# Optimization experiments

Measured on AMD Instinct MI355X. Metric: run time of the kernel, lower is better.

## Reference

```python
import jax, jax.numpy as jnp
import numpy as np

RANK_W, SP_W, ANS_W = 1.0, 1.0, 1.0


def _listmle(thres, scores, labels):
    # thres [B,1], scores [B,P], labels [B,P] with values in {-1,0,1}
    fs = jnp.concatenate([thres, scores], axis=1)                      # [B,K]
    fl = jnp.concatenate([jnp.full_like(thres, 0.5), labels], axis=1)  # [B,K]
    s = jnp.exp(fs) * (fl != -1.0).astype(fs.dtype)
    # rest[b,j] = sum_k s[b,k] * (fl[b,k] < fl[b,j])  (sorting in the original
    # is only used to enumerate; with the 0.5 break it reduces to masking
    # entries with label >= 0.5)
    less = (fl[:, None, :] < fl[:, :, None]).astype(fs.dtype)          # [B,j,k]
    rest = jnp.einsum('bjk,bk->bj', less, s)
    mask = fl >= 0.5
    den = jnp.where(mask, s + rest, 1.0)
    logp = jnp.where(mask, fs - jnp.log(den), 0.0)  # log(s_j/(s_j+rest)) with s_j=exp(fs_j)
    return -jnp.sum(logp)


def setup_inputs() -> dict:
    key = jax.random.key(0)
    B, S, H, NS, NP, A = 8, 4096, 1024, 64, 32, 8
    ks = jax.random.split(key, 12)
    sequence_output = jax.random.normal(ks[0], (B, S, H), jnp.float32)
    token_type_ids = jax.random.randint(ks[1], (B, S), 0, 2).astype(jnp.int32)
    # strictly increasing sentence boundaries; last 4 sentences padded with -1
    base = jnp.round(jnp.linspace(8, S - 8, NS + 1)).astype(jnp.int32)
    sent_starts = jnp.broadcast_to(base, (B, NS + 1)).copy()
    sent_starts = sent_starts.at[:, -4:].set(-1)
    para_starts = jnp.sort(jax.random.randint(ks[2], (B, NP), 0, S), axis=1).astype(jnp.int32)
    para_labels = jax.random.randint(ks[3], (B, NP), -1, 2).astype(jnp.float32)
    sp_sent_labels = jax.random.randint(ks[4], (B, NS), -1, 2).astype(jnp.float32)
    starts = jax.random.randint(ks[5], (B, A), -1, S).astype(jnp.int32)
    ends = jax.random.randint(ks[6], (B, A), -1, S).astype(jnp.int32)
    Wqa = jax.random.normal(ks[7], (H, 2), jnp.float32) * 0.02
    bqa = jnp.zeros((2,), jnp.float32)
    Wrank = jax.random.normal(ks[8], (H, 1), jnp.float32) * 0.02
    brank = jnp.zeros((1,), jnp.float32)
    Wsp = jax.random.normal(ks[9], (H, 1), jnp.float32) * 0.02
    bsp = jnp.zeros((1,), jnp.float32)
    return {"sequence_output": sequence_output, "token_type_ids": token_type_ids,
            "sent_starts": sent_starts, "para_starts": para_starts,
            "para_labels": para_labels, "sp_sent_labels": sp_sent_labels,
            "starts": starts, "ends": ends, "Wqa": Wqa, "bqa": bqa,
            "Wrank": Wrank, "brank": brank, "Wsp": Wsp, "bsp": bsp}


def reference(sequence_output, token_type_ids, sent_starts, para_starts,
              para_labels, sp_sent_labels, starts, ends,
              Wqa, bqa, Wrank, brank, Wsp, bsp):
    B, S, H = sequence_output.shape
    logits = sequence_output @ Wqa + bqa                               # [B,S,2]
    tt1 = token_type_ids == 1
    start_logits = jnp.where(tt1, logits[..., 0], -jnp.inf)
    end_logits = jnp.where(tt1, logits[..., 1], -jnp.inf)

    rank_thres = sequence_output[:, 0, :] @ Wrank + brank              # [B,1]
    sent_thres = sequence_output[:, 0, :] @ Wsp + bsp                  # [B,1]

    # ragged per-sentence mean pooling via prefix sums
    csum = jnp.concatenate([jnp.zeros((B, 1, H), sequence_output.dtype),
                            jnp.cumsum(sequence_output, axis=1)], axis=1)  # [B,S+1,H]
    st = sent_starts[:, :-1]
    en = sent_starts[:, 1:]
    valid = en != -1                                                   # [B,NS]
    st_c = jnp.clip(st, 0, S)
    en_c = jnp.maximum(jnp.clip(en, 0, S), st_c + 1)
    NS = st.shape[1]
    g_en = jnp.take_along_axis(csum, jnp.broadcast_to(en_c[:, :, None], (B, NS, H)), axis=1)
    g_st = jnp.take_along_axis(csum, jnp.broadcast_to(st_c[:, :, None], (B, NS, H)), axis=1)
    seg_mean = (g_en - g_st) / (en_c - st_c)[:, :, None].astype(sequence_output.dtype)
    sent_rep = jnp.where(valid[:, :, None], seg_mean, sequence_output[:, -1:, :])
    sp_score = (sent_rep @ Wsp + bsp)[..., 0]                          # [B,NS]

    NP = para_starts.shape[1]
    para_rep = jnp.take_along_axis(
        sequence_output, jnp.broadcast_to(para_starts[:, :, None].astype(jnp.int32), (B, NP, H)), axis=1)
    para_score = (para_rep @ Wrank + brank)[..., 0]                    # [B,NP]

    rank_loss = _listmle(rank_thres, para_score, para_labels)
    sp_loss = _listmle(sent_thres, sp_score, sp_sent_labels)

    ls_start = jax.nn.log_softmax(start_logits, axis=-1)
    ls_end = jax.nn.log_softmax(end_logits, axis=-1)

    def ce(ls, tgt):  # CrossEntropy with ignore_index=-1, reduction='none'
        safe = jnp.clip(tgt, 0, S - 1)
        nll = -jnp.take_along_axis(ls, safe, axis=1)
        return jnp.where(tgt == -1, 0.0, nll)

    loss_tensor = ce(ls_start, starts) + ce(ls_end, ends)              # [B,A]
    lp = -loss_tensor
    lp = jnp.where(lp == 0.0, -jnp.inf, lp)
    m = jnp.sum(jnp.exp(lp), axis=1)                                   # [B]
    pos = m > 0
    span_loss = -jnp.sum(jnp.where(pos, jnp.log(jnp.where(pos, m, 1.0)), 0.0))

    loss = rank_loss * RANK_W + span_loss * ANS_W + sp_loss * SP_W
    return (loss, rank_loss * RANK_W, sp_loss * SP_W)
```

## Files before the change

kernel.cpp:

```cpp
#include <hip/hip_runtime.h>
#include <math.h>

#define B 8
#define S 4096
#define H 1024
#define NSEG 64
#define NPARA 32
#define NA 8
#define BS (B * S)
#define PAD(i) ((i) + ((i) >> 4))
#define ROWS_PER_BLK 16
#define GROUPS 4
#define BLKS_PER_B (S / ROWS_PER_BLK)
#define NBLK (B * BLKS_PER_B)

__device__ __forceinline__ void gload_lds16(const float4* g, float4* l)
{
    __builtin_amdgcn_global_load_lds(
        (const __attribute__((address_space(1))) void*)g,
        (__attribute__((address_space(3))) void*)l, 16, 0, 0);
}

__device__ __forceinline__ float2 lse_merge(float2 A, float2 Bv)
{
    float m = fmaxf(A.x, Bv.x);
    float s = 0.f;
    if (A.y > 0.f)  s += A.y * expf(A.x - m);
    if (Bv.y > 0.f) s += Bv.y * expf(Bv.x - m);
    return make_float2(m, s);
}

__global__ __launch_bounds__(256) void dots_kernel(
    const float4* __restrict__ seq4,
    const float*  __restrict__ Wqa,
    const float*  __restrict__ Wsp,
    const float*  __restrict__ Wrank,
    const int*    __restrict__ tt,
    float4* __restrict__ sc4,
    float4* __restrict__ lse_part,
    float*  __restrict__ out)
{
    const int blk   = blockIdx.x;
    const int b     = blk >> 8;
    const int rbase = (blk & 255) * ROWS_PER_BLK;
    const int t     = threadIdx.x;
    const int w     = t >> 6, lane = t & 63;

    if (blk == 0 && t == 0) { out[0] = 0.f; out[1] = 0.f; out[2] = 0.f; }

    __shared__ float4 sbuf[2][1024];
    __shared__ float4 lsep[4];

    float wq0[4][4], wq1[4][4];
    float4 wspv[4], wrkv[4];
#pragma unroll
    for (int c = 0; c < 4; ++c) {
        int h0 = (lane + 64 * c) * 4;
#pragma unroll
        for (int j = 0; j < 4; ++j) {
            wq0[c][j] = Wqa[(h0 + j) * 2 + 0];
            wq1[c][j] = Wqa[(h0 + j) * 2 + 1];
        }
        wspv[c] = *(const float4*)(Wsp + h0);
        wrkv[c] = *(const float4*)(Wrank + h0);
    }

    const size_t baseF4 = (size_t)(b * S + rbase) * (H / 4);
    const int    wbase  = t & ~63;

    {
        const float4* gsrc = seq4 + baseF4;
#pragma unroll
        for (int k = 0; k < 4; ++k)
            gload_lds16(gsrc + k * 256 + t, &sbuf[0][k * 256 + wbase]);
    }
    __syncthreads();

    const int* ttb = tt + b * S;
    float m0 = -INFINITY, s0 = 0.f, m1 = -INFINITY, s1 = 0.f;

    for (int g = 0; g < GROUPS; ++g) {
        if (g + 1 < GROUPS) {
            const float4* gsrc = seq4 + baseF4 + (size_t)(g + 1) * (4 * H / 4);
#pragma unroll
            for (int k = 0; k < 4; ++k)
                gload_lds16(gsrc + k * 256 + t, &sbuf[(g + 1) & 1][k * 256 + wbase]);
        }
        const float4* rowp = &sbuf[g & 1][w * 256];
        float a0 = 0.f, a1 = 0.f, a2 = 0.f, a3 = 0.f;
#pragma unroll
        for (int c = 0; c < 4; ++c) {
            float4 v = rowp[lane + 64 * c];
            a0 += v.x * wq0[c][0] + v.y * wq0[c][1] + v.z * wq0[c][2] + v.w * wq0[c][3];
            a1 += v.x * wq1[c][0] + v.y * wq1[c][1] + v.z * wq1[c][2] + v.w * wq1[c][3];
            a2 += v.x * wspv[c].x + v.y * wspv[c].y + v.z * wspv[c].z + v.w * wspv[c].w;
            a3 += v.x * wrkv[c].x + v.y * wrkv[c].y + v.z * wrkv[c].z + v.w * wrkv[c].w;
        }
#pragma unroll
        for (int off = 32; off > 0; off >>= 1) {
            a0 += __shfl_xor(a0, off);
            a1 += __shfl_xor(a1, off);
            a2 += __shfl_xor(a2, off);
            a3 += __shfl_xor(a3, off);
        }
        const int srow = rbase + g * 4 + w;
        if (ttb[srow] == 1) {
            float mn = fmaxf(m0, a0);
            s0 = s0 * expf(m0 - mn) + expf(a0 - mn); m0 = mn;
            mn = fmaxf(m1, a1);
            s1 = s1 * expf(m1 - mn) + expf(a1 - mn); m1 = mn;
        }
        if (lane == 0)
            sc4[b * S + srow] = make_float4(a0, a1, a2, a3);
        __syncthreads();
    }

    if (lane == 0) lsep[w] = make_float4(m0, s0, m1, s1);
    __syncthreads();
    if (t == 0) {
        float2 L0 = make_float2(lsep[0].x, lsep[0].y);
        float2 L1 = make_float2(lsep[0].z, lsep[0].w);
#pragma unroll
        for (int i = 1; i < 4; ++i) {
            L0 = lse_merge(L0, make_float2(lsep[i].x, lsep[i].y));
            L1 = lse_merge(L1, make_float2(lsep[i].z, lsep[i].w));
        }
        lse_part[blk] = make_float4(L0.x, L0.y, L1.x, L1.y);
    }
}

__device__ __forceinline__ float blk_reduce1(float v, float* wred1, int t)
{
    const int lane = t & 63, w = t >> 6;
#pragma unroll
    for (int off = 32; off > 0; off >>= 1) v += __shfl_xor(v, off);
    if (lane == 0) wred1[w] = v;
    __syncthreads();
    float r = wred1[0] + wred1[1] + wred1[2] + wred1[3];
    __syncthreads();
    return r;
}

__device__ float listmle_block(const float* fs, const float* fl, float* se,
                               int n, float* wred1, int t)
{
    if (t < n) se[t] = (fl[t] != -1.0f) ? expf(fs[t]) : 0.0f;
    __syncthreads();
    float lp = 0.0f;
    if (t < n && fl[t] >= 0.5f) {
        float fj = fl[t];
        float rest = 0.0f;
        for (int k = 0; k < n; ++k)
            if (fl[k] < fj) rest += se[k];
        lp = fs[t] - logf(se[t] + rest);
    }
    float tot = blk_reduce1(lp, wred1, t);
    return -tot;
}

__global__ __launch_bounds__(256) void batch_kernel(
    const float4* __restrict__ sc4,
    const float4* __restrict__ lse_part,
    const int*    __restrict__ tt,
    const int*    __restrict__ sent_starts,
    const int*    __restrict__ para_starts,
    const float*  __restrict__ para_labels,
    const float*  __restrict__ sp_labels,
    const int*    __restrict__ starts,
    const int*    __restrict__ ends,
    float* __restrict__ out)
{
    const int b = blockIdx.x;
    const int t = threadIdx.x;
    const int lane = t & 63, w = t >> 6;

    __shared__ float  a[PAD(S) + 1];
    __shared__ float4 lsew[4];
    __shared__ float  wred1[4];
    __shared__ float  fsb[1 + NSEG], flb[1 + NSEG], seb[1 + NSEG];
    __shared__ float  lse_sh[2];

    const float4* sb  = sc4 + (size_t)b * S;
    const int*    ttb = tt + b * S;

    {
        float4 P = lse_part[b * BLKS_PER_B + t];
        float2 L0 = make_float2(P.x, P.y);
        float2 L1 = make_float2(P.z, P.w);
#pragma unroll
        for (int off = 32; off > 0; off >>= 1) {
            float2 O0 = make_float2(__shfl_xor(L0.x, off), __shfl_xor(L0.y, off));
            float2 O1 = make_float2(__shfl_xor(L1.x, off), __shfl_xor(L1.y, off));
            L0 = lse_merge(L0, O0);
            L1 = lse_merge(L1, O1);
        }
        if (lane == 0) lsew[w] = make_float4(L0.x, L0.y, L1.x, L1.y);
        __syncthreads();
        if (t == 0) {
            float2 M0 = make_float2(lsew[0].x, lsew[0].y);
            float2 M1 = make_float2(lsew[0].z, lsew[0].w);
#pragma unroll
            for (int i = 1; i < 4; ++i) {
                M0 = lse_merge(M0, make_float2(lsew[i].x, lsew[i].y));
                M1 = lse_merge(M1, make_float2(lsew[i].z, lsew[i].w));
            }
            lse_sh[0] = M0.x + logf(M0.y);
            lse_sh[1] = M1.x + logf(M1.y);
        }
    }

    {
        for (int s = t; s < S; s += 256) a[PAD(s)] = sb[s].z;
        __syncthreads();
        float vals[16];
        float run = 0.f;
        const int base = t * 16;
#pragma unroll
        for (int i = 0; i < 16; ++i) {
            run += a[PAD(base + i)];
            vals[i] = run;
        }
        float v = run;
#pragma unroll
        for (int off = 1; off < 64; off <<= 1) {
            float u = __shfl_up(v, off, 64);
            if (lane >= off) v += u;
        }
        if (lane == 63) wred1[w] = v;
        __syncthreads();
        float woff = 0.f;
        for (int i = 0; i < w; ++i) woff += wred1[i];
        const float excl = woff + v - run;
        __syncthreads();
#pragma unroll
        for (int i = 0; i < 16; ++i) a[PAD(base + i + 1)] = excl + vals[i];
        if (t == 0) a[PAD(0)] = 0.f;
        __syncthreads();
    }

    if (t == 0) { fsb[0] = sb[0].z; flb[0] = 0.5f; }
    if (t < NSEG) {
        int st = sent_starts[b * (NSEG + 1) + t];
        int en = sent_starts[b * (NSEG + 1) + t + 1];
        int stc = min(max(st, 0), S);
        int enc = max(min(max(en, 0), S), stc + 1);
        float score;
        if (en != -1) {
            int encc = min(enc, S);
            score = (a[PAD(encc)] - a[PAD(stc)]) / (float)(enc - stc);
        } else {
            score = sb[S - 1].z;
        }
        fsb[1 + t] = score;
        flb[1 + t] = sp_labels[b * NSEG + t];
    }
    __syncthreads();
    float sp_loss_b = listmle_block(fsb, flb, seb, 1 + NSEG, wred1, t);

    if (t == 0) { fsb[0] = sb[0].w; flb[0] = 0.5f; }
    if (t < NPARA) {
        int ps = para_starts[b * NPARA + t];
        fsb[1 + t] = sb[ps].w;
        flb[1 + t] = para_labels[b * NPARA + t];
    }
    __syncthreads();
    float rank_loss_b = listmle_block(fsb, flb, seb, 1 + NPARA, wred1, t);

    float e_a = 0.f;
    if (t < NA) {
        const float lse0 = lse_sh[0], lse1 = lse_sh[1];
        int tsv = starts[b * NA + t];
        int tev = ends[b * NA + t];
        float lt = 0.f;
        if (tsv != -1) {
            int sf = min(max(tsv, 0), S - 1);
            float sl = (ttb[sf] == 1) ? sb[sf].x : -INFINITY;
            lt += -(sl - lse0);
        }
        if (tev != -1) {
            int sf = min(max(tev, 0), S - 1);
            float el = (ttb[sf] == 1) ? sb[sf].y : -INFINITY;
            lt += -(el - lse1);
        }
        float lp = -lt;
        e_a = (lp == 0.0f) ? 0.f : expf(lp);
    }
#pragma unroll
    for (int off = 4; off > 0; off >>= 1) e_a += __shfl_xor(e_a, off, 8);
    if (t == 0) {
        float logm = (e_a > 0.f) ? logf(e_a) : 0.f;
        atomicAdd(out + 0, rank_loss_b + sp_loss_b - logm);
        atomicAdd(out + 1, rank_loss_b);
        atomicAdd(out + 2, sp_loss_b);
    }
}

extern "C" void kernel_launch(void* const* d_in, const int* in_sizes, int n_in,
                              void* d_out, int out_size, void* d_ws, size_t ws_size,
                              hipStream_t stream)
{
    const float* seq         = (const float*)d_in[0];
    const int*   tt          = (const int*)  d_in[1];
    const int*   sent_starts = (const int*)  d_in[2];
    const int*   para_starts = (const int*)  d_in[3];
    const float* para_labels = (const float*)d_in[4];
    const float* sp_labels   = (const float*)d_in[5];
    const int*   starts      = (const int*)  d_in[6];
    const int*   ends        = (const int*)  d_in[7];
    const float* Wqa         = (const float*)d_in[8];
    const float* Wrank       = (const float*)d_in[10];
    const float* Wsp         = (const float*)d_in[12];

    float*  out      = (float*)d_out;
    float4* sc4      = (float4*)d_ws;
    float4* lse_part = sc4 + (size_t)BS;

    dots_kernel<<<NBLK, 256, 0, stream>>>((const float4*)seq, Wqa, Wsp, Wrank,
                                          tt, sc4, lse_part, out);
    batch_kernel<<<B, 256, 0, stream>>>(sc4, lse_part, tt, sent_starts,
                                        para_starts, para_labels, sp_labels,
                                        starts, ends, out);
}
```

Baseline: 40.82 us.

## Fuse segment sums into dots kernel and load rows via registers

The dots kernel now loads rows straight into registers with double buffering, replacing the async global-to-LDS copies and per-group barriers. Each block now covers 32 rows instead of 16. It maps each row to its sentence segment and emits per-block partial segment sums, so the batch kernel no longer needs its 4096-element prefix scan in LDS and only accumulates partials with shared atomics. This shortens the serial single-block-per-batch tail, at the cost of a small per-block segment search. It assumes each 32-row block spans at most two segments.

New measurement: 46.04 us. 1.13x slower.

```diff
diff --git a/kernel.cpp b/kernel.cpp
--- a/kernel.cpp
+++ b/kernel.cpp
@@ -8,18 +8,9 @@
 #define NPARA 32
 #define NA 8
 #define BS (B * S)
-#define PAD(i) ((i) + ((i) >> 4))
-#define ROWS_PER_BLK 16
-#define GROUPS 4
+#define ROWS_PER_BLK 32
 #define BLKS_PER_B (S / ROWS_PER_BLK)
 #define NBLK (B * BLKS_PER_B)
-
-__device__ __forceinline__ void gload_lds16(const float4* g, float4* l)
-{
-    __builtin_amdgcn_global_load_lds(
-        (const __attribute__((address_space(1))) void*)g,
-        (__attribute__((address_space(3))) void*)l, 16, 0, 0);
-}
 
 __device__ __forceinline__ float2 lse_merge(float2 A, float2 Bv)
 {
@@ -32,69 +23,91 @@
 
 __global__ __launch_bounds__(256) void dots_kernel(
     const float4* __restrict__ seq4,
-    const float*  __restrict__ Wqa,
-    const float*  __restrict__ Wsp,
-    const float*  __restrict__ Wrank,
+    const float4* __restrict__ Wqa4,
+    const float4* __restrict__ Wsp4,
+    const float4* __restrict__ Wrank4,
     const int*    __restrict__ tt,
+    const int*    __restrict__ sent_starts,
     float4* __restrict__ sc4,
     float4* __restrict__ lse_part,
+    float4* __restrict__ segpart,
     float*  __restrict__ out)
 {
     const int blk   = blockIdx.x;
-    const int b     = blk >> 8;
-    const int rbase = (blk & 255) * ROWS_PER_BLK;
+    const int b     = blk >> 7;
+    const int rbase = (blk & 127) * ROWS_PER_BLK;
     const int t     = threadIdx.x;
     const int w     = t >> 6, lane = t & 63;
 
     if (blk == 0 && t == 0) { out[0] = 0.f; out[1] = 0.f; out[2] = 0.f; }
 
-    __shared__ float4 sbuf[2][1024];
+    __shared__ int    ssh[NSEG + 1];
+    __shared__ int    rowseg[ROWS_PER_BLK];
+    __shared__ int    ttsh[ROWS_PER_BLK];
+    __shared__ float2 wacc[4];
     __shared__ float4 lsep[4];
-
-    float wq0[4][4], wq1[4][4];
-    float4 wspv[4], wrkv[4];
+    __shared__ int    jlo_sh;
+
+    float4 qA[4], qB[4], spv[4], rkv[4];
 #pragma unroll
     for (int c = 0; c < 4; ++c) {
-        int h0 = (lane + 64 * c) * 4;
-#pragma unroll
-        for (int j = 0; j < 4; ++j) {
-            wq0[c][j] = Wqa[(h0 + j) * 2 + 0];
-            wq1[c][j] = Wqa[(h0 + j) * 2 + 1];
-        }
-        wspv[c] = *(const float4*)(Wsp + h0);
-        wrkv[c] = *(const float4*)(Wrank + h0);
-    }
-
-    const size_t baseF4 = (size_t)(b * S + rbase) * (H / 4);
-    const int    wbase  = t & ~63;
-
-    {
-        const float4* gsrc = seq4 + baseF4;
-#pragma unroll
-        for (int k = 0; k < 4; ++k)
-            gload_lds16(gsrc + k * 256 + t, &sbuf[0][k * 256 + wbase]);
-    }
-    __syncthreads();
-
-    const int* ttb = tt + b * S;
+        const int ch = lane + 64 * c;
+        qA[c]  = Wqa4[ch * 2];
+        qB[c]  = Wqa4[ch * 2 + 1];
+        spv[c] = Wsp4[ch];
+        rkv[c] = Wrank4[ch];
+    }
+
+    if (t < NSEG + 1) ssh[t] = sent_starts[b * (NSEG + 1) + t];
+    __syncthreads();
+    if (t < ROWS_PER_BLK) {
+        ttsh[t] = tt[b * S + rbase + t];
+        const int r = rbase + t;
+        int j = -1;
+        for (int k = 0; k < NSEG; ++k) {
+            int en = ssh[k + 1];
+            if (en == -1) break;
+            if (r >= ssh[k] && r < en) { j = k; break; }
+        }
+        rowseg[t] = j;
+    }
+    __syncthreads();
+    if (t == 0) {
+        int jl = -1;
+        for (int i = 0; i < ROWS_PER_BLK; ++i)
+            if (rowseg[i] >= 0) { jl = rowseg[i]; break; }
+        jlo_sh = jl;
+    }
+    __syncthreads();
+    const int jlo = jlo_sh;
+
+    const float4* base = seq4 + (size_t)(b * S + rbase) * (H / 4);
+    float4 bufA[4], bufB[4];
+#pragma unroll
+    for (int c = 0; c < 4; ++c)
+        bufA[c] = base[(size_t)w * 256 + lane + 64 * c];
+
     float m0 = -INFINITY, s0 = 0.f, m1 = -INFINITY, s1 = 0.f;
-
-    for (int g = 0; g < GROUPS; ++g) {
-        if (g + 1 < GROUPS) {
-            const float4* gsrc = seq4 + baseF4 + (size_t)(g + 1) * (4 * H / 4);
-#pragma unroll
-            for (int k = 0; k < 4; ++k)
-                gload_lds16(gsrc + k * 256 + t, &sbuf[(g + 1) & 1][k * 256 + wbase]);
-        }
-        const float4* rowp = &sbuf[g & 1][w * 256];
+    float sA = 0.f, sB = 0.f;
+
+#pragma unroll
+    for (int g = 0; g < 8; ++g) {
+        const float4* cur = (g & 1) ? bufB : bufA;
+        float4*       nxt = (g & 1) ? bufA : bufB;
+        if (g + 1 < 8) {
+            const int nr = (g + 1) * 4 + w;
+#pragma unroll
+            for (int c = 0; c < 4; ++c)
+                nxt[c] = base[(size_t)nr * 256 + lane + 64 * c];
+        }
         float a0 = 0.f, a1 = 0.f, a2 = 0.f, a3 = 0.f;
 #pragma unroll
         for (int c = 0; c < 4; ++c) {
-            float4 v = rowp[lane + 64 * c];
-            a0 += v.x * wq0[c][0] + v.y * wq0[c][1] + v.z * wq0[c][2] + v.w * wq0[c][3];
-            a1 += v.x * wq1[c][0] + v.y * wq1[c][1] + v.z * wq1[c][2] + v.w * wq1[c][3];
-            a2 += v.x * wspv[c].x + v.y * wspv[c].y + v.z * wspv[c].z + v.w * wspv[c].w;
-            a3 += v.x * wrkv[c].x + v.y * wrkv[c].y + v.z * wrkv[c].z + v.w * wrkv[c].w;
+            float4 v = cur[c];
+            a0 += v.x * qA[c].x + v.y * qA[c].z + v.z * qB[c].x + v.w * qB[c].z;
+            a1 += v.x * qA[c].y + v.y * qA[c].w + v.z * qB[c].y + v.w * qB[c].w;
+            a2 += v.x * spv[c].x + v.y * spv[c].y + v.z * spv[c].z + v.w * spv[c].w;
+            a3 += v.x * rkv[c].x + v.y * rkv[c].y + v.z * rkv[c].z + v.w * rkv[c].w;
         }
 #pragma unroll
         for (int off = 32; off > 0; off >>= 1) {
@@ -103,29 +116,34 @@
             a2 += __shfl_xor(a2, off);
             a3 += __shfl_xor(a3, off);
         }
-        const int srow = rbase + g * 4 + w;
-        if (ttb[srow] == 1) {
+        const int lrow = g * 4 + w;
+        const int srow = rbase + lrow;
+        if (ttsh[lrow] == 1) {
             float mn = fmaxf(m0, a0);
             s0 = s0 * expf(m0 - mn) + expf(a0 - mn); m0 = mn;
             mn = fmaxf(m1, a1);
             s1 = s1 * expf(m1 - mn) + expf(a1 - mn); m1 = mn;
         }
+        const int j = rowseg[lrow];
+        if (j >= 0) { if (j == jlo) sA += a2; else sB += a2; }
         if (lane == 0)
-            sc4[b * S + srow] = make_float4(a0, a1, a2, a3);
-        __syncthreads();
-    }
-
-    if (lane == 0) lsep[w] = make_float4(m0, s0, m1, s1);
+            sc4[(size_t)b * S + srow] = make_float4(a0, a1, a2, a3);
+    }
+
+    if (lane == 0) { lsep[w] = make_float4(m0, s0, m1, s1); wacc[w] = make_float2(sA, sB); }
     __syncthreads();
     if (t == 0) {
         float2 L0 = make_float2(lsep[0].x, lsep[0].y);
         float2 L1 = make_float2(lsep[0].z, lsep[0].w);
+        float SA = wacc[0].x, SB = wacc[0].y;
 #pragma unroll
         for (int i = 1; i < 4; ++i) {
             L0 = lse_merge(L0, make_float2(lsep[i].x, lsep[i].y));
             L1 = lse_merge(L1, make_float2(lsep[i].z, lsep[i].w));
+            SA += wacc[i].x; SB += wacc[i].y;
         }
         lse_part[blk] = make_float4(L0.x, L0.y, L1.x, L1.y);
+        segpart[blk]  = make_float4(__int_as_float(jlo), SA, SB, 0.f);
     }
 }
 
@@ -161,6 +179,7 @@
 __global__ __launch_bounds__(256) void batch_kernel(
     const float4* __restrict__ sc4,
     const float4* __restrict__ lse_part,
+    const float4* __restrict__ segpart,
     const int*    __restrict__ tt,
     const int*    __restrict__ sent_starts,
     const int*    __restrict__ para_starts,
@@ -174,8 +193,9 @@
     const int t = threadIdx.x;
     const int lane = t & 63, w = t >> 6;
 
-    __shared__ float  a[PAD(S) + 1];
-    __shared__ float4 lsew[4];
+    __shared__ float4 lsew[2];
+    __shared__ float  segsum[NSEG + 2];
+    __shared__ int    ssh[NSEG + 1];
     __shared__ float  wred1[4];
     __shared__ float  fsb[1 + NSEG], flb[1 + NSEG], seb[1 + NSEG];
     __shared__ float  lse_sh[2];
@@ -183,7 +203,11 @@
     const float4* sb  = sc4 + (size_t)b * S;
     const int*    ttb = tt + b * S;
 
-    {
+    if (t < NSEG + 2) segsum[t] = 0.f;
+    if (t < NSEG + 1) ssh[t] = sent_starts[b * (NSEG + 1) + t];
+    __syncthreads();
+
+    if (t < BLKS_PER_B) {
         float4 P = lse_part[b * BLKS_PER_B + t];
         float2 L0 = make_float2(P.x, P.y);
         float2 L1 = make_float2(P.z, P.w);
@@ -195,59 +219,33 @@
             L1 = lse_merge(L1, O1);
         }
         if (lane == 0) lsew[w] = make_float4(L0.x, L0.y, L1.x, L1.y);
-        __syncthreads();
-        if (t == 0) {
-            float2 M0 = make_float2(lsew[0].x, lsew[0].y);
-            float2 M1 = make_float2(lsew[0].z, lsew[0].w);
-#pragma unroll
-            for (int i = 1; i < 4; ++i) {
-                M0 = lse_merge(M0, make_float2(lsew[i].x, lsew[i].y));
-                M1 = lse_merge(M1, make_float2(lsew[i].z, lsew[i].w));
-            }
-            lse_sh[0] = M0.x + logf(M0.y);
-            lse_sh[1] = M1.x + logf(M1.y);
-        }
-    }
-
-    {
-        for (int s = t; s < S; s += 256) a[PAD(s)] = sb[s].z;
-        __syncthreads();
-        float vals[16];
-        float run = 0.f;
-        const int base = t * 16;
-#pragma unroll
-        for (int i = 0; i < 16; ++i) {
-            run += a[PAD(base + i)];
-            vals[i] = run;
-        }
-        float v = run;
-#pragma unroll
-        for (int off = 1; off < 64; off <<= 1) {
-            float u = __shfl_up(v, off, 64);
-            if (lane >= off) v += u;
-        }
-        if (lane == 63) wred1[w] = v;
-        __syncthreads();
-        float woff = 0.f;
-        for (int i = 0; i < w; ++i) woff += wred1[i];
-        const float excl = woff + v - run;
-        __syncthreads();
-#pragma unroll
-        for (int i = 0; i < 16; ++i) a[PAD(base + i + 1)] = excl + vals[i];
-        if (t == 0) a[PAD(0)] = 0.f;
-        __syncthreads();
+
+        float4 SP = segpart[b * BLKS_PER_B + t];
+        int jl = __float_as_int(SP.x);
+        if (jl >= 0) {
+            atomicAdd(&segsum[jl], SP.y);
+            atomicAdd(&segsum[jl + 1], SP.z);
+        }
+    }
+    __syncthreads();
+    if (t == 0) {
+        float2 M0 = lse_merge(make_float2(lsew[0].x, lsew[0].y),
+                              make_float2(lsew[1].x, lsew[1].y));
+        float2 M1 = lse_merge(make_float2(lsew[0].z, lsew[0].w),
+                              make_float2(lsew[1].z, lsew[1].w));
+        lse_sh[0] = M0.x + logf(M0.y);
+        lse_sh[1] = M1.x + logf(M1.y);
     }
 
     if (t == 0) { fsb[0] = sb[0].z; flb[0] = 0.5f; }
     if (t < NSEG) {
-        int st = sent_starts[b * (NSEG + 1) + t];
-        int en = sent_starts[b * (NSEG + 1) + t + 1];
-        int stc = min(max(st, 0), S);
-        int enc = max(min(max(en, 0), S), stc + 1);
+        int st = ssh[t];
+        int en = ssh[t + 1];
         float score;
         if (en != -1) {
-            int encc = min(enc, S);
-            score = (a[PAD(encc)] - a[PAD(stc)]) / (float)(enc - stc);
+            int stc = min(max(st, 0), S);
+            int enc = max(min(max(en, 0), S), stc + 1);
+            score = segsum[t] / (float)(enc - stc);
         } else {
             score = sb[S - 1].z;
         }
@@ -314,10 +312,15 @@
     float*  out      = (float*)d_out;
     float4* sc4      = (float4*)d_ws;
     float4* lse_part = sc4 + (size_t)BS;
-
-    dots_kernel<<<NBLK, 256, 0, stream>>>((const float4*)seq, Wqa, Wsp, Wrank,
-                                          tt, sc4, lse_part, out);
-    batch_kernel<<<B, 256, 0, stream>>>(sc4, lse_part, tt, sent_starts,
+    float4* segpart  = lse_part + NBLK;
+
+    dots_kernel<<<NBLK, 256, 0, stream>>>((const float4*)seq,
+                                          (const float4*)Wqa,
+                                          (const float4*)Wsp,
+                                          (const float4*)Wrank,
+                                          tt, sent_starts,
+                                          sc4, lse_part, segpart, out);
+    batch_kernel<<<B, 256, 0, stream>>>(sc4, lse_part, segpart, tt, sent_starts,
                                         para_starts, para_labels, sp_labels,
                                         starts, ends, out);
 }
```
